# Kernel tuning notes

Hardware: AMD Instinct MI355X
Metric: run time of the kernel (lower is better)

Reference implementation:

```python
import jax, jax.numpy as jnp
import numpy as np

B, T, D = 8, 4096, 512
EXPAND = 2
DI = D * EXPAND          # d_inner = 1024
K = 7                    # d_conv
LN_EPS = 1e-5


def setup_inputs() -> dict:
    key = jax.random.key(0)
    ks = jax.random.split(key, 12)
    s = 0.02
    return {
        "x": jax.random.normal(ks[0], (B, T, D), dtype=jnp.float32),
        # shared input projection (no bias): weight (2*DI, D), torch Linear layout
        "in_proj_w": jax.random.normal(ks[1], (2 * DI, D), dtype=jnp.float32) * s,
        # forward Conv1DSequenceMixer: depthwise conv (DI,1,K) + bias, proj Linear (DI,DI)+bias
        "conv_fwd_w": jax.random.normal(ks[2], (DI, 1, K), dtype=jnp.float32) * s,
        "conv_fwd_b": jnp.zeros((DI,), dtype=jnp.float32),
        "proj_fwd_w": jax.random.normal(ks[3], (DI, DI), dtype=jnp.float32) * s,
        "proj_fwd_b": jnp.zeros((DI,), dtype=jnp.float32),
        # backward Conv1DSequenceMixer
        "conv_bwd_w": jax.random.normal(ks[4], (DI, 1, K), dtype=jnp.float32) * s,
        "conv_bwd_b": jnp.zeros((DI,), dtype=jnp.float32),
        "proj_bwd_w": jax.random.normal(ks[5], (DI, DI), dtype=jnp.float32) * s,
        "proj_bwd_b": jnp.zeros((DI,), dtype=jnp.float32),
        # diagonal term and gate scale
        "diag_weight": jnp.full((DI,), 0.1, dtype=jnp.float32),
        "gate_scale": jnp.full((1,), 0.5, dtype=jnp.float32),
        # output projection (no bias): (D, DI)
        "out_proj_w": jax.random.normal(ks[6], (D, DI), dtype=jnp.float32) * s,
        # LayerNorm
        "ln_g": jnp.ones((D,), dtype=jnp.float32),
        "ln_b": jnp.zeros((D,), dtype=jnp.float32),
    }


def _seq_mixer(x, conv_w, conv_b, proj_w, proj_b):
    """Conv1DSequenceMixer: causal depthwise conv + SiLU(Linear). x: (B,T,C)."""
    C = x.shape[-1]
    # torch pads both sides by K-1 then truncates to T -> equivalent to causal left-pad
    xp = jnp.pad(x, ((0, 0), (K - 1, 0), (0, 0)))            # (B, T+K-1, C)
    y = jax.lax.conv_general_dilated(
        xp.transpose(0, 2, 1), conv_w, window_strides=(1,), padding="VALID",
        dimension_numbers=("NCH", "OIH", "NCH"), feature_group_count=C,
    )                                                         # (B, C, T)
    y = y.transpose(0, 2, 1) + conv_b                         # (B, T, C)
    y = jnp.einsum("btc,oc->bto", y, proj_w) + proj_b
    return jax.nn.silu(y)


def _shift_right(x):
    """Shift one step right along time, zero-padding the first step."""
    return jnp.pad(x, ((0, 0), (1, 0), (0, 0)))[:, :-1, :]


def reference(x, in_proj_w, conv_fwd_w, conv_fwd_b, proj_fwd_w, proj_fwd_b,
              conv_bwd_w, conv_bwd_b, proj_bwd_w, proj_bwd_b,
              diag_weight, gate_scale, out_proj_w, ln_g, ln_b):
    residual = x
    xz = jnp.einsum("btd,ed->bte", x, in_proj_w)              # (B,T,2*DI)
    x_proj, z = xz[..., :DI], xz[..., DI:]

    y_fwd = _shift_right(_seq_mixer(x_proj, conv_fwd_w, conv_fwd_b, proj_fwd_w, proj_fwd_b))

    x_flip = jnp.flip(x_proj, axis=1)
    y_bwd = _shift_right(_seq_mixer(x_flip, conv_bwd_w, conv_bwd_b, proj_bwd_w, proj_bwd_b))
    y_bwd = jnp.flip(y_bwd, axis=1)

    y = y_fwd + y_bwd + x_proj * diag_weight                  # quasiseparable sum
    y = y * jax.nn.silu(z) * gate_scale                       # SiLU gate + scale
    y = jnp.einsum("bte,de->btd", y, out_proj_w)              # out_proj (no bias)

    h = residual + y                                          # dropout=0 (eval)
    mu = jnp.mean(h, axis=-1, keepdims=True)
    var = jnp.var(h, axis=-1, keepdims=True)
    return (h - mu) * jax.lax.rsqrt(var + LN_EPS) * ln_g + ln_b
```

## Files before the change

kernel.cpp:

```cpp
#include <hip/hip_runtime.h>
#include <hip/hip_bf16.h>
#include <cstdint>

#define T_SEQ  4096
#define DMODEL 512
#define DINNER 1024
#define MTOT   32768

typedef __bf16 bf16_t;
typedef bf16_t bf16x8 __attribute__((ext_vector_type(8)));
typedef bf16_t bf16x4v __attribute__((ext_vector_type(4)));
typedef float  f32x4  __attribute__((ext_vector_type(4)));

__device__ __forceinline__ void async_copy16(const bf16_t* g, bf16_t* l) {
  __builtin_amdgcn_global_load_lds(
      (const __attribute__((address_space(1))) void*)g,
      (__attribute__((address_space(3))) void*)l,
      16, 0, 0);
}

__device__ __forceinline__ float silu_f(float v) {
  return v / (1.f + __expf(-v));
}

__device__ __forceinline__ int xcd_swizzle_flat() {
  const int nwg = gridDim.x * gridDim.y;
  const int orig = blockIdx.y * gridDim.x + blockIdx.x;
  const int q = nwg >> 3, r = nwg & 7;
  const int xcd = orig & 7, lid = orig >> 3;
  return (xcd < r ? xcd * (q + 1) : r * (q + 1) + (xcd - r) * q) + lid;
}

__global__ __launch_bounds__(256) void cast_kernel(
    const float* __restrict__ s, bf16_t* __restrict__ d, int n4)
{
  const int i = blockIdx.x * 256 + threadIdx.x;
  if (i < n4) {
    const f32x4 v = ((const f32x4*)s)[i];
    bf16x4v o;
    o[0] = (bf16_t)v[0]; o[1] = (bf16_t)v[1];
    o[2] = (bf16_t)v[2]; o[3] = (bf16_t)v[3];
    ((bf16x4v*)d)[i] = o;
  }
}

__global__ __launch_bounds__(256) void wtr_kernel(
    const float* __restrict__ w, float* __restrict__ wt)
{
  const int i = blockIdx.x * 256 + threadIdx.x;
  if (i < 7 * DINNER) {
    const int c = i & (DINNER - 1);
    const int k = i >> 10;
    wt[i] = w[c * 7 + k];
  }
}

template <int EPI>
__global__ __launch_bounds__(256, 3) void gemm_bt(
    const bf16_t* __restrict__ A, const bf16_t* __restrict__ B,
    bf16_t* __restrict__ Cb, float* __restrict__ Cf,
    const float* __restrict__ resid,
    int N, int K)
{
  constexpr int BM = 128, BN = 128, BK = 64;
  __shared__ __attribute__((aligned(16))) bf16_t sA[BM * BK];
  __shared__ __attribute__((aligned(16))) bf16_t sB[BN * BK];

  const int tid  = threadIdx.x;
  const int bflat = xcd_swizzle_flat();
  const int m0 = (bflat / gridDim.x) * BM;
  const int n0 = (bflat % gridDim.x) * BN;

  const int w    = tid >> 6, lane = tid & 63;
  const int wm   = (w & 1) << 6, wn = (w >> 1) << 6;
  const int quad = lane >> 4, lrow = lane & 15;

  f32x4 acc[4][4] = {};

  for (int kt = 0; kt < K; kt += BK) {
    __syncthreads();
#pragma unroll
    for (int i = 0; i < 4; ++i) {
      const int f = (i * 256 + tid) << 3;
      const int r = f >> 6, c = f & 63;
      async_copy16(&A[(size_t)(m0 + r) * K + kt + c], &sA[f]);
      async_copy16(&B[(size_t)(n0 + r) * K + kt + c], &sB[f]);
    }
    __syncthreads();
#pragma unroll
    for (int ks = 0; ks < 2; ++ks) {
      const int ko = ks * 32 + (quad << 3);
      bf16x8 av[4], bv[4];
#pragma unroll
      for (int i = 0; i < 4; ++i) {
        av[i] = *(const bf16x8*)&sA[(wm + i * 16 + lrow) * BK + ko];
        bv[i] = *(const bf16x8*)&sB[(wn + i * 16 + lrow) * BK + ko];
      }
#pragma unroll
      for (int mi = 0; mi < 4; ++mi)
#pragma unroll
        for (int ni = 0; ni < 4; ++ni)
          acc[mi][ni] = __builtin_amdgcn_mfma_f32_16x16x32_bf16(
              av[mi], bv[ni], acc[mi][ni], 0, 0, 0);
    }
  }

#pragma unroll
  for (int mi = 0; mi < 4; ++mi)
#pragma unroll
    for (int ni = 0; ni < 4; ++ni)
#pragma unroll
      for (int r = 0; r < 4; ++r) {
        const int row = m0 + wm + mi * 16 + (quad << 2) + r;
        const int col = n0 + wn + ni * 16 + lrow;
        float v = acc[mi][ni][r];
        if constexpr (EPI == 0) {
          Cb[(size_t)row * N + col] = (bf16_t)v;
        } else {
          v += resid[(size_t)row * N + col];
          Cf[(size_t)row * N + col] = v;
        }
      }
}

__global__ __launch_bounds__(256, 2) void gemm_dual(
    const bf16_t* __restrict__ A1, const bf16_t* __restrict__ A2,
    const bf16_t* __restrict__ B1, const bf16_t* __restrict__ B2,
    const float* __restrict__ b1, const float* __restrict__ b2,
    const bf16_t* __restrict__ xzc, const float* __restrict__ diag,
    const float* __restrict__ gs, bf16_t* __restrict__ G,
    int r0, int loc0, int N, int K)
{
  constexpr int BM = 128, BN = 128, BK = 64;
  __shared__ __attribute__((aligned(16))) bf16_t sA1[BM * BK];
  __shared__ __attribute__((aligned(16))) bf16_t sA2[BM * BK];
  __shared__ __attribute__((aligned(16))) bf16_t sB1[BN * BK];
  __shared__ __attribute__((aligned(16))) bf16_t sB2[BN * BK];

  const int tid  = threadIdx.x;
  const int bflat = xcd_swizzle_flat();
  const int m0 = (bflat / gridDim.x) * BM;
  const int n0 = (bflat % gridDim.x) * BN;

  const int w    = tid >> 6, lane = tid & 63;
  const int wm   = (w & 1) << 6, wn = (w >> 1) << 6;
  const int quad = lane >> 4, lrow = lane & 15;

  f32x4 accf[4][4] = {};
  f32x4 accb[4][4] = {};

  for (int kt = 0; kt < K; kt += BK) {
    __syncthreads();
#pragma unroll
    for (int i = 0; i < 4; ++i) {
      const int f = (i * 256 + tid) << 3;
      const int r = f >> 6, c = f & 63;
      const size_t ga = (size_t)(m0 + r) * K + kt + c;
      const size_t gb = (size_t)(n0 + r) * K + kt + c;
      async_copy16(&A1[ga], &sA1[f]);
      async_copy16(&A2[ga], &sA2[f]);
      async_copy16(&B1[gb], &sB1[f]);
      async_copy16(&B2[gb], &sB2[f]);
    }
    __syncthreads();
#pragma unroll
    for (int ks = 0; ks < 2; ++ks) {
      const int ko = ks * 32 + (quad << 3);
      bf16x8 av[4], bv[4];
#pragma unroll
      for (int i = 0; i < 4; ++i) {
        av[i] = *(const bf16x8*)&sA1[(wm + i * 16 + lrow) * BK + ko];
        bv[i] = *(const bf16x8*)&sB1[(wn + i * 16 + lrow) * BK + ko];
      }
#pragma unroll
      for (int mi = 0; mi < 4; ++mi)
#pragma unroll
        for (int ni = 0; ni < 4; ++ni)
          accf[mi][ni] = __builtin_amdgcn_mfma_f32_16x16x32_bf16(
              av[mi], bv[ni], accf[mi][ni], 0, 0, 0);
#pragma unroll
      for (int i = 0; i < 4; ++i) {
        av[i] = *(const bf16x8*)&sA2[(wm + i * 16 + lrow) * BK + ko];
        bv[i] = *(const bf16x8*)&sB2[(wn + i * 16 + lrow) * BK + ko];
      }
#pragma unroll
      for (int mi = 0; mi < 4; ++mi)
#pragma unroll
        for (int ni = 0; ni < 4; ++ni)
          accb[mi][ni] = __builtin_amdgcn_mfma_f32_16x16x32_bf16(
              av[mi], bv[ni], accb[mi][ni], 0, 0, 0);
    }
  }

  const float gsv = gs[0];
  int   colv[4];
  float b1v[4], b2v[4], dgv[4];
#pragma unroll
  for (int ni = 0; ni < 4; ++ni) {
    const int col = n0 + wn + ni * 16 + lrow;
    colv[ni] = col;
    b1v[ni] = b1[col];
    b2v[ni] = b2[col];
    dgv[ni] = diag[col];
  }
#pragma unroll
  for (int mi = 0; mi < 4; ++mi)
#pragma unroll
    for (int r = 0; r < 4; ++r) {
      const int row = m0 + wm + mi * 16 + (quad << 2) + r;
      const int t = (row + r0) & (T_SEQ - 1);
      const bool tf = (t > 0), tb = (t < T_SEQ - 1);
      const bf16_t* xrow = &xzc[(size_t)(loc0 + row) * 2048];
#pragma unroll
      for (int ni = 0; ni < 4; ++ni) {
        const float sf = silu_f(accf[mi][ni][r] + b1v[ni]);
        const float sb = silu_f(accb[mi][ni][r] + b2v[ni]);
        const float xp = (float)xrow[colv[ni]];
        const float z  = (float)xrow[colv[ni] + DINNER];
        float y = xp * dgv[ni];
        if (tf) y += sf;
        if (tb) y += sb;
        G[(size_t)row * N + colv[ni]] = (bf16_t)(y * silu_f(z) * gsv);
      }
    }
}

template <int DIR>
__global__ __launch_bounds__(256) void conv_kernel(
    const bf16_t* __restrict__ xzc,
    const float* __restrict__ wt, const float* __restrict__ bc,
    bf16_t* __restrict__ vout, int r0, int loc0, int Mc)
{
  const int idx = blockIdx.x * 256 + threadIdx.x;
  const int c8  = idx & 127;
  const int tg  = idx >> 7;
  const int bt0 = tg << 2;
  const int t0  = (bt0 + r0) & (T_SEQ - 1);
  const int lt0 = bt0 + loc0;
  const int cc  = c8 << 3;

  float wv[7][8];
#pragma unroll
  for (int k = 0; k < 7; ++k) {
    const f32x4 a = *(const f32x4*)&wt[k * DINNER + cc];
    const f32x4 b = *(const f32x4*)&wt[k * DINNER + cc + 4];
#pragma unroll
    for (int u = 0; u < 4; ++u) { wv[k][u] = a[u]; wv[k][u + 4] = b[u]; }
  }

  float acc[4][8];
  {
    const f32x4 a = *(const f32x4*)&bc[cc];
    const f32x4 b = *(const f32x4*)&bc[cc + 4];
#pragma unroll
    for (int i = 0; i < 4; ++i)
#pragma unroll
      for (int u = 0; u < 4; ++u) { acc[i][u] = a[u]; acc[i][u + 4] = b[u]; }
  }

#pragma unroll
  for (int rr = 0; rr < 10; ++rr) {
    int lt = (DIR == 0) ? (lt0 - 7 + rr) : (lt0 + 1 + rr);
    lt = lt < 0 ? 0 : (lt > Mc - 1 ? Mc - 1 : lt);
    const bf16x8 xv = *(const bf16x8*)&xzc[(size_t)lt * 2048 + cc];
    float xf[8];
#pragma unroll
    for (int u = 0; u < 8; ++u) xf[u] = (float)xv[u];
#pragma unroll
    for (int i = 0; i < 4; ++i) {
      const int k = (DIR == 0) ? (rr - i) : (i + 6 - rr);
      if (k >= 0 && k <= 6) {
        const bool ok = (DIR == 0) ? (t0 + i >= 7 - k)
                                   : (t0 + i <= (T_SEQ - 8) + k);
        if (ok) {
#pragma unroll
          for (int u = 0; u < 8; ++u) acc[i][u] += wv[k][u] * xf[u];
        }
      }
    }
  }

#pragma unroll
  for (int i = 0; i < 4; ++i) {
    bf16x8 o;
#pragma unroll
    for (int u = 0; u < 8; ++u) o[u] = (bf16_t)acc[i][u];
    *(bf16x8*)&vout[(size_t)(bt0 + i) * DINNER + cc] = o;
  }
}

__global__ __launch_bounds__(256) void ln_kernel(
    const float* __restrict__ h,
    const float* __restrict__ lng, const float* __restrict__ lnb,
    float* __restrict__ out, int r0)
{
  const int row = blockIdx.x;
  const int tid = threadIdx.x;
  const float* hr = h + (size_t)row * DMODEL;
  const float v0 = hr[tid], v1 = hr[tid + 256];
  float s  = v0 + v1;
  float ss = v0 * v0 + v1 * v1;
#pragma unroll
  for (int off = 1; off < 64; off <<= 1) {
    s  += __shfl_xor(s, off);
    ss += __shfl_xor(ss, off);
  }
  __shared__ float ps[8];
  const int w = tid >> 6;
  if ((tid & 63) == 0) { ps[w] = s; ps[w + 4] = ss; }
  __syncthreads();
  s  = ps[0] + ps[1] + ps[2] + ps[3];
  ss = ps[4] + ps[5] + ps[6] + ps[7];
  const float mu  = s * (1.f / DMODEL);
  const float inv = rsqrtf(ss * (1.f / DMODEL) - mu * mu + 1e-5f);
  float* o = out + (size_t)(r0 + row) * DMODEL;
  o[tid]       = (v0 - mu) * inv * lng[tid]       + lnb[tid];
  o[tid + 256] = (v1 - mu) * inv * lng[tid + 256] + lnb[tid + 256];
}

extern "C" void kernel_launch(void* const* d_in, const int* in_sizes, int n_in,
                              void* d_out, int out_size, void* d_ws, size_t ws_size,
                              hipStream_t stream) {
  const float* x    = (const float*)d_in[0];
  const float* in_w = (const float*)d_in[1];
  const float* cfw  = (const float*)d_in[2];
  const float* cfb  = (const float*)d_in[3];
  const float* pfw  = (const float*)d_in[4];
  const float* pfb  = (const float*)d_in[5];
  const float* cbw  = (const float*)d_in[6];
  const float* cbb  = (const float*)d_in[7];
  const float* pbw  = (const float*)d_in[8];
  const float* pbb  = (const float*)d_in[9];
  const float* diag = (const float*)d_in[10];
  const float* gs   = (const float*)d_in[11];
  const float* ow   = (const float*)d_in[12];
  const float* lng  = (const float*)d_in[13];
  const float* lnb  = (const float*)d_in[14];
  float* out = (float*)d_out;

  char* ws = (char*)d_ws;

  bf16_t* xw   = (bf16_t*)(ws);
  bf16_t* inwb = (bf16_t*)(ws + (size_t)33554432);
  bf16_t* pfwb = (bf16_t*)(ws + (size_t)35651584);
  bf16_t* pbwb = (bf16_t*)(ws + (size_t)37748736);
  bf16_t* owb  = (bf16_t*)(ws + (size_t)39845888);
  float*  wtf  = (float*)(ws + (size_t)40894464);
  float*  wtb  = (float*)(ws + (size_t)40923136);
  const size_t persist = 40951808;

  int CH = 128;
  {
    const int cands[9] = {32768, 16384, 8192, 4096, 2048, 1024, 512, 256, 128};
    for (int i = 0; i < 9; ++i) {
      const size_t req = persist + (size_t)(cands[i] + 256) * 4096 +
                         (size_t)3 * cands[i] * 2048;
      if (ws_size >= req) { CH = cands[i]; break; }
    }
  }

  char* cb = ws + persist;
  const size_t xz_cap = (size_t)(CH + 256) * 4096;
  bf16_t* xzc  = (bf16_t*)cb;
  bf16_t* bufA = (bf16_t*)(cb + xz_cap);
  bf16_t* bufB = (bf16_t*)(cb + xz_cap + (size_t)CH * 2048);
  bf16_t* bufC = (bf16_t*)(cb + xz_cap + (size_t)CH * 4096);
  float*  hbuf = (float*)cb;

  dim3 blk(256);

  cast_kernel<<<dim3(16384), blk, 0, stream>>>(x,    xw,   4194304);
  cast_kernel<<<dim3(1024),  blk, 0, stream>>>(in_w, inwb, 262144);
  cast_kernel<<<dim3(1024),  blk, 0, stream>>>(pfw,  pfwb, 262144);
  cast_kernel<<<dim3(1024),  blk, 0, stream>>>(pbw,  pbwb, 262144);
  cast_kernel<<<dim3(512),   blk, 0, stream>>>(ow,   owb,  131072);
  wtr_kernel<<<dim3(28), blk, 0, stream>>>(cfw, wtf);
  wtr_kernel<<<dim3(28), blk, 0, stream>>>(cbw, wtb);

  for (int r0 = 0; r0 < MTOT; r0 += CH) {
    const int g0 = (r0 >= 128) ? (r0 - 128) : 0;
    int g1 = r0 + CH + 128; if (g1 > MTOT) g1 = MTOT;
    const int Mc   = g1 - g0;
    const int loc0 = r0 - g0;

    gemm_bt<0><<<dim3(2048 / 128, Mc / 128), blk, 0, stream>>>(
        xw + (size_t)g0 * 512, inwb, xzc, nullptr, nullptr, 2048, 512);

    conv_kernel<0><<<dim3(CH / 8), blk, 0, stream>>>(
        xzc, wtf, cfb, bufA, r0, loc0, Mc);

    conv_kernel<1><<<dim3(CH / 8), blk, 0, stream>>>(
        xzc, wtb, cbb, bufB, r0, loc0, Mc);

    gemm_dual<<<dim3(1024 / 128, CH / 128), blk, 0, stream>>>(
        bufA, bufB, pfwb, pbwb, pfb, pbb, xzc, diag, gs, bufC,
        r0, loc0, 1024, 1024);

    gemm_bt<2><<<dim3(512 / 128, CH / 128), blk, 0, stream>>>(
        bufC, owb, nullptr, hbuf, x + (size_t)r0 * 512, 512, 1024);

    ln_kernel<<<dim3(CH), blk, 0, stream>>>(hbuf, lng, lnb, out, r0);
  }
}
```

Baseline: 648.8 us.

## Double-buffer LDS tiles in bf16 GEMM to overlap global loads with MFMA

```diff
diff --git a/kernel.cpp b/kernel.cpp
--- a/kernel.cpp
+++ b/kernel.cpp
@@ -56,15 +56,17 @@
 }
 
 template <int EPI>
-__global__ __launch_bounds__(256, 3) void gemm_bt(
+__global__ __launch_bounds__(256, 2) void gemm_bt(
     const bf16_t* __restrict__ A, const bf16_t* __restrict__ B,
     bf16_t* __restrict__ Cb, float* __restrict__ Cf,
     const float* __restrict__ resid,
     int N, int K)
 {
   constexpr int BM = 128, BN = 128, BK = 64;
-  __shared__ __attribute__((aligned(16))) bf16_t sA[BM * BK];
-  __shared__ __attribute__((aligned(16))) bf16_t sB[BN * BK];
+  __shared__ __attribute__((aligned(16))) bf16_t sA0[BM * BK];
+  __shared__ __attribute__((aligned(16))) bf16_t sB0[BN * BK];
+  __shared__ __attribute__((aligned(16))) bf16_t sA1[BM * BK];
+  __shared__ __attribute__((aligned(16))) bf16_t sB1[BN * BK];
 
   const int tid  = threadIdx.x;
   const int bflat = xcd_swizzle_flat();
@@ -75,26 +77,30 @@
   const int wm   = (w & 1) << 6, wn = (w >> 1) << 6;
   const int quad = lane >> 4, lrow = lane & 15;
 
+  const int f0 = tid << 3;
+  const int sr = f0 >> 6, sc = f0 & 63;
+
   f32x4 acc[4][4] = {};
 
-  for (int kt = 0; kt < K; kt += BK) {
-    __syncthreads();
+  auto STAGE = [&](int kt, bf16_t* dA, bf16_t* dB) {
 #pragma unroll
     for (int i = 0; i < 4; ++i) {
-      const int f = (i * 256 + tid) << 3;
-      const int r = f >> 6, c = f & 63;
-      async_copy16(&A[(size_t)(m0 + r) * K + kt + c], &sA[f]);
-      async_copy16(&B[(size_t)(n0 + r) * K + kt + c], &sB[f]);
-    }
-    __syncthreads();
+      const int f = f0 + (i << 11);
+      const int r = sr + (i << 5);
+      async_copy16(&A[(size_t)(m0 + r) * K + kt + sc], &dA[f]);
+      async_copy16(&B[(size_t)(n0 + r) * K + kt + sc], &dB[f]);
+    }
+  };
+
+  auto COMPUTE = [&](const bf16_t* cA, const bf16_t* cB) {
 #pragma unroll
     for (int ks = 0; ks < 2; ++ks) {
       const int ko = ks * 32 + (quad << 3);
       bf16x8 av[4], bv[4];
 #pragma unroll
       for (int i = 0; i < 4; ++i) {
-        av[i] = *(const bf16x8*)&sA[(wm + i * 16 + lrow) * BK + ko];
-        bv[i] = *(const bf16x8*)&sB[(wn + i * 16 + lrow) * BK + ko];
+        av[i] = *(const bf16x8*)&cA[(wm + i * 16 + lrow) * BK + ko];
+        bv[i] = *(const bf16x8*)&cB[(wn + i * 16 + lrow) * BK + ko];
       }
 #pragma unroll
       for (int mi = 0; mi < 4; ++mi)
@@ -103,6 +109,18 @@
           acc[mi][ni] = __builtin_amdgcn_mfma_f32_16x16x32_bf16(
               av[mi], bv[ni], acc[mi][ni], 0, 0, 0);
     }
+  };
+
+  STAGE(0, sA0, sB0);
+  __syncthreads();
+
+  for (int kt = 0; kt < K; kt += 2 * BK) {
+    if (kt + BK < K) STAGE(kt + BK, sA1, sB1);
+    COMPUTE(sA0, sB0);
+    __syncthreads();
+    if (kt + 2 * BK < K) STAGE(kt + 2 * BK, sA0, sB0);
+    COMPUTE(sA1, sB1);
+    __syncthreads();
   }
 
 #pragma unroll
```

Measured after the change: 641.8 us. No clear change (-1.1%).
